# Kernel optimization log

Measured on AMD Instinct MI355X. Metric: run time of the kernel, lower is better.

## Reference

```python
import jax, jax.numpy as jnp
import numpy as np

B, N, D, H, S = 64, 1000, 512, 8, 20
DK = D // H
TANH_CLIP = 10.0
NEG = -1e9


def setup_inputs() -> dict:
    key = jax.random.key(0)
    k1, k2, k3, k4, k5 = jax.random.split(key, 5)
    embeddings = jax.random.normal(k1, (B, N, D), dtype=jnp.float32)
    q = jax.random.normal(k2, (B, S, D), dtype=jnp.float32)
    # action_mask: True = feasible. Ensure at least one feasible node per row.
    action_mask = jax.random.bernoulli(k3, 0.5, (B, S, N))
    action_mask = action_mask.at[:, :, 0].set(True)
    W_kvl = jax.random.normal(k4, (D, 3 * D), dtype=jnp.float32) * (1.0 / np.sqrt(D))
    W_out = jax.random.normal(k5, (D, D), dtype=jnp.float32) * (1.0 / np.sqrt(D))
    return {"embeddings": embeddings, "q": q, "action_mask": action_mask,
            "W_kvl": W_kvl, "W_out": W_out}


def reference(embeddings, q, action_mask, W_kvl, W_out):
    # _precompute: project node embeddings into glimpse K, V and logit K
    kvl = jnp.einsum('bnd,de->bne', embeddings, W_kvl)  # [B,N,3D]
    glimpse_k, glimpse_v, logit_k = jnp.split(kvl, 3, axis=-1)
    # dynamic embedding is zero (StaticEmbedding for TSP)

    mask = ~action_mask  # True = infeasible, shape [B,S,N]

    # multi-head glimpse attention
    qh = q.reshape(B, S, H, DK)
    kh = glimpse_k.reshape(B, N, H, DK)
    vh = glimpse_v.reshape(B, N, H, DK)
    compat = jnp.einsum('bshd,bnhd->bhsn', qh, kh) / np.sqrt(DK)
    compat = jnp.where(mask[:, None, :, :], NEG, compat)
    attn = jax.nn.softmax(compat, axis=-1)
    heads = jnp.einsum('bhsn,bnhd->bshd', attn, vh).reshape(B, S, D)
    glimpse = jnp.einsum('bsd,de->bse', heads, W_out)  # [B,S,D]

    # pointer logits against logit_k, tanh clipping, mask, log-softmax
    logits = jnp.einsum('bsd,bnd->bsn', glimpse, logit_k) / np.sqrt(D)
    logits = TANH_CLIP * jnp.tanh(logits)
    logits = jnp.where(mask, NEG, logits)
    log_p = jax.nn.log_softmax(logits, axis=-1)  # [B,S,N]

    # rearrange 'b s l -> (s b) l'
    return jnp.swapaxes(log_p, 0, 1).reshape(S * B, N)
```

## Files before the change

### kernel.cpp

```cpp
#include <hip/hip_runtime.h>

#define BB 64
#define NN 1000
#define NP 1024
#define DD 512
#define HH 8
#define SS 20
#define NEGV -1e9f

typedef float v4f __attribute__((ext_vector_type(4)));
typedef short v8s __attribute__((ext_vector_type(8)));
typedef int   v8i __attribute__((ext_vector_type(8)));
typedef int   v4i __attribute__((ext_vector_type(4)));
typedef unsigned char uchar;
typedef unsigned long long ulong_t;

static __device__ __forceinline__ short f2bf(float f) {
    unsigned u = __builtin_bit_cast(unsigned, f);
    u = (u + 0x7fffu + ((u >> 16) & 1u)) >> 16;
    return (short)u;
}
static __device__ __forceinline__ float bf2f(short s) {
    unsigned u = ((unsigned)(unsigned short)s) << 16;
    return __builtin_bit_cast(float, u);
}
static __device__ __forceinline__ uchar f2fp8(float f) {
    return (uchar)(__builtin_amdgcn_cvt_pk_fp8_f32(f, 0.f, 0, false) & 0xff);
}

static __device__ __forceinline__ void gld16(const void* g, void* l) {
    __builtin_amdgcn_global_load_lds(
        (const __attribute__((address_space(1))) void*)(g),
        (__attribute__((address_space(3))) void*)(l),
        16, 0, 0);
}

__global__ void transpose_bf16(const float* __restrict__ src, short* __restrict__ dst,
                               int R, int C) {
    __shared__ float t[32][33];
    int c0 = blockIdx.x * 32, r0 = blockIdx.y * 32;
    int x = threadIdx.x & 31, y = threadIdx.x >> 5;
    for (int k = 0; k < 32; k += 8)
        t[y + k][x] = src[(long)(r0 + y + k) * C + c0 + x];
    __syncthreads();
    for (int k = 0; k < 32; k += 8)
        dst[(long)(c0 + y + k) * R + r0 + x] = f2bf(t[x][y + k]);
}

__global__ void transpose_fp8(const float* __restrict__ src, uchar* __restrict__ dst,
                              int R, int C) {
    __shared__ float t[32][33];
    int c0 = blockIdx.x * 32, r0 = blockIdx.y * 32;
    int x = threadIdx.x & 31, y = threadIdx.x >> 5;
    for (int k = 0; k < 32; k += 8)
        t[y + k][x] = src[(long)(r0 + y + k) * C + c0 + x];
    __syncthreads();
    for (int k = 0; k < 32; k += 8)
        dst[(long)(c0 + y + k) * R + r0 + x] = f2fp8(t[x][y + k]);
}

__global__ void cvt_fp8(const float* __restrict__ src, int* __restrict__ dst, int n8) {
    int i = blockIdx.x * 256 + threadIdx.x;
    if (i >= n8) return;
    long o = (long)i * 8;
    v4f a = *(const v4f*)(src + o);
    v4f b = *(const v4f*)(src + o + 4);
    int lo = __builtin_amdgcn_cvt_pk_fp8_f32(a.x, a.y, 0, false);
    lo = __builtin_amdgcn_cvt_pk_fp8_f32(a.z, a.w, lo, true);
    int hi = __builtin_amdgcn_cvt_pk_fp8_f32(b.x, b.y, 0, false);
    hi = __builtin_amdgcn_cvt_pk_fp8_f32(b.z, b.w, hi, true);
    int2 r; r.x = lo; r.y = hi;
    *(int2*)(dst + i * 2) = r;
}

__global__ __launch_bounds__(256) void gemm_kvl(const uchar* __restrict__ emb8,
                                                const uchar* __restrict__ Wt8,
                                                uchar* __restrict__ kvl8) {
    __shared__ __align__(16) uchar As[128 * 128];
    __shared__ __align__(16) uchar Bs[128 * 128];
    __shared__ __align__(16) short rp[4 * 16 * 72];
    int tid = threadIdx.x;
    int id = blockIdx.x;
    int m_idx, n_idx;
    if (id < 5952) { int g = id / 96, r = id % 96; m_idx = g * 8 + (r & 7); n_idx = r >> 3; }
    else { int t = id - 5952; m_idx = 496 + (t & 3); n_idx = t >> 2; }
    int n0 = n_idx * 128, m0 = m_idx * 128;
    int wid = tid >> 6, lane = tid & 63, quad = lane >> 4, l16 = lane & 15;
    int wm = wid & 1, wn = wid >> 1;
    v4f acc[4][4] = {};
    const uchar* Ag = emb8 + (long)m0 * 512;
    const uchar* Bg = Wt8 + (long)n0 * 512;
    int rsub = lane >> 3;
    int kc = ((lane & 7) ^ rsub) * 16;
    for (int kk = 0; kk < 512; kk += 128) {
        #pragma unroll
        for (int p = 0; p < 4; ++p) {
            int rl = wid * 32 + p * 8;
            gld16(Ag + (long)(rl + rsub) * 512 + kk + kc, As + rl * 128);
            gld16(Bg + (long)(rl + rsub) * 512 + kk + kc, Bs + rl * 128);
        }
        __syncthreads();
        v8i af[4], bf[4];
        #pragma unroll
        for (int i = 0; i < 4; ++i) {
            int m = wm * 64 + i * 16 + l16;
            int c0 = (quad * 2) ^ (m & 7), c1 = (quad * 2 + 1) ^ (m & 7);
            v4i lo = *(const v4i*)(As + m * 128 + c0 * 16);
            v4i hi = *(const v4i*)(As + m * 128 + c1 * 16);
            af[i] = __builtin_shufflevector(lo, hi, 0, 1, 2, 3, 4, 5, 6, 7);
        }
        #pragma unroll
        for (int j = 0; j < 4; ++j) {
            int n = wn * 64 + j * 16 + l16;
            int c0 = (quad * 2) ^ (n & 7), c1 = (quad * 2 + 1) ^ (n & 7);
            v4i lo = *(const v4i*)(Bs + n * 128 + c0 * 16);
            v4i hi = *(const v4i*)(Bs + n * 128 + c1 * 16);
            bf[j] = __builtin_shufflevector(lo, hi, 0, 1, 2, 3, 4, 5, 6, 7);
        }
        #pragma unroll
        for (int i = 0; i < 4; ++i)
            #pragma unroll
            for (int j = 0; j < 4; ++j)
                acc[i][j] = __builtin_amdgcn_mfma_scale_f32_16x16x128_f8f6f4(
                    af[i], bf[j], acc[i][j], 0, 0, 0, 0x7f7f7f7f, 0, 0x7f7f7f7f);
        __syncthreads();
    }
    short* r = rp + wid * (16 * 72);
    #pragma unroll
    for (int i = 0; i < 4; ++i) {
        #pragma unroll
        for (int j = 0; j < 4; ++j)
            #pragma unroll
            for (int rr = 0; rr < 4; ++rr)
                r[(quad * 4 + rr) * 72 + j * 16 + l16] = f2bf(acc[i][j][rr]);
        #pragma unroll
        for (int h = 0; h < 2; ++h) {
            int rowl = h * 8 + (lane >> 3);
            int colc = (lane & 7) * 8;
            v8s val = *(const v8s*)(r + rowl * 72 + colc);
            int lo = __builtin_amdgcn_cvt_pk_fp8_f32(bf2f(val[0]), bf2f(val[1]), 0, false);
            lo = __builtin_amdgcn_cvt_pk_fp8_f32(bf2f(val[2]), bf2f(val[3]), lo, true);
            int hi = __builtin_amdgcn_cvt_pk_fp8_f32(bf2f(val[4]), bf2f(val[5]), 0, false);
            hi = __builtin_amdgcn_cvt_pk_fp8_f32(bf2f(val[6]), bf2f(val[7]), hi, true);
            int2 st; st.x = lo; st.y = hi;
            *(int2*)(kvl8 + (long)(m0 + wm * 64 + i * 16 + rowl) * 1536 +
                     n0 + wn * 64 + colc) = st;
        }
    }
}

__global__ void transpose_v(const uchar* __restrict__ kvl8, uchar* __restrict__ Vt8) {
    int bh = blockIdx.x, b = bh >> 3, h = bh & 7;
    int n0 = blockIdx.y * 64;
    __shared__ uchar T[64][72];
    int tid = threadIdx.x;
    #pragma unroll
    for (int it = 0; it < 2; ++it) {
        int nl = (tid >> 3) + it * 32;
        int n = n0 + nl;
        int nc = n < NN ? n : NN - 1;
        int d0 = (tid & 7) * 8;
        ulong_t v = *(const ulong_t*)(kvl8 + ((long)b * NN + nc) * 1536 + DD + h * 64 + d0);
        uchar* vb = (uchar*)&v;
        #pragma unroll
        for (int j = 0; j < 8; ++j) T[d0 + j][nl] = vb[j];
    }
    __syncthreads();
    #pragma unroll
    for (int it = 0; it < 2; ++it) {
        int d = (tid >> 3) + it * 32;
        int ns = (tid & 7) * 8;
        *(ulong_t*)(Vt8 + ((long)bh * 64 + d) * NP + n0 + ns) = *(const ulong_t*)&T[d][ns];
    }
}

#define CST 1036
__global__ __launch_bounds__(256) void attn_fused(const float* __restrict__ q,
                                                  const uchar* __restrict__ kvl8,
                                                  const uchar* __restrict__ Vt8,
                                                  const int* __restrict__ mask,
                                                  float* __restrict__ heads) {
    int b = blockIdx.x, h = blockIdx.y;
    __shared__ __align__(16) uchar qs[32 * 72];
    __shared__ __align__(16) short cmp[SS * CST];
    int tid = threadIdx.x, wid = tid >> 6, lane = tid & 63, quad = lane >> 4, l16 = lane & 15;
    for (int i = tid; i < 32 * 64; i += 256) {
        int row = i >> 6, col = i & 63;
        float v = (row < SS) ? q[((long)b * SS + row) * DD + h * 64 + col] : 0.f;
        qs[row * 72 + col] = f2fp8(v);
    }
    __syncthreads();
    long af[2][2];
    #pragma unroll
    for (int mt = 0; mt < 2; ++mt)
        #pragma unroll
        for (int ks = 0; ks < 2; ++ks)
            af[mt][ks] = *(const long*)(qs + (mt * 16 + l16) * 72 + ks * 32 + quad * 8);
    for (int t = 0; t < 16; ++t) {
        int nt = wid * 16 + t;
        int n = nt * 16 + l16;
        int nc = n < NN ? n : NN - 1;
        const uchar* kp = kvl8 + ((long)b * NN + nc) * 1536 + h * 64 + quad * 8;
        long b0 = *(const long*)kp;
        long b1 = *(const long*)(kp + 32);
        #pragma unroll
        for (int mt = 0; mt < 2; ++mt) {
            v4f a = {};
            a = __builtin_amdgcn_mfma_f32_16x16x32_fp8_fp8(af[mt][0], b0, a, 0, 0, 0);
            a = __builtin_amdgcn_mfma_f32_16x16x32_fp8_fp8(af[mt][1], b1, a, 0, 0, 0);
            #pragma unroll
            for (int r = 0; r < 4; ++r) {
                int s = mt * 16 + quad * 4 + r;
                if (s < SS) cmp[s * CST + nt * 16 + l16] = f2bf(a[r] * 0.125f);
            }
        }
    }
    __syncthreads();
    for (int s = wid; s < SS; s += 4) {
        const int* mr = mask + ((long)b * SS + s) * NN;
        float x[16];
        float mx = NEGV;
        #pragma unroll
        for (int i = 0; i < 16; ++i) {
            int n = lane + 64 * i;
            float v = bf2f(cmp[s * CST + n]);
            bool feas = (n < NN) && (mr[n < NN ? n : 0] != 0);
            x[i] = feas ? v : NEGV;
            mx = fmaxf(mx, x[i]);
        }
        for (int off = 32; off; off >>= 1) mx = fmaxf(mx, __shfl_xor(mx, off));
        float sum = 0.f;
        #pragma unroll
        for (int i = 0; i < 16; ++i) { x[i] = __expf(x[i] - mx); sum += x[i]; }
        for (int off = 32; off; off >>= 1) sum += __shfl_xor(sum, off);
        float inv = 1.0f / sum;
        uchar* pr = (uchar*)cmp + (long)s * (CST * 2);
        #pragma unroll
        for (int i = 0; i < 16; ++i) pr[lane + 64 * i] = f2fp8(x[i] * inv);
    }
    __syncthreads();
    int mt = wid & 1, dt0 = (wid >> 1) * 2;
    int srow = mt * 16 + l16; if (srow > SS - 1) srow = SS - 1;
    const uchar* ap = (const uchar*)cmp + (long)srow * (CST * 2) + quad * 8;
    const uchar* vb = Vt8 + (long)(b * HH + h) * 64 * NP;
    v4f acc[2] = {};
    for (int k0 = 0; k0 < NP; k0 += 32) {
        long afr = *(const long*)(ap + k0);
        #pragma unroll
        for (int i = 0; i < 2; ++i) {
            long bfr = *(const long*)(vb + (long)((dt0 + i) * 16 + l16) * NP + k0 + quad * 8);
            acc[i] = __builtin_amdgcn_mfma_f32_16x16x32_fp8_fp8(afr, bfr, acc[i], 0, 0, 0);
        }
    }
    #pragma unroll
    for (int i = 0; i < 2; ++i)
        #pragma unroll
        for (int r = 0; r < 4; ++r) {
            int s = mt * 16 + quad * 4 + r;
            if (s < SS)
                heads[((long)b * SS + s) * DD + h * 64 + (dt0 + i) * 16 + l16] = acc[i][r];
        }
}

__global__ __launch_bounds__(256) void out_proj(const float* __restrict__ heads,
                                                const short* __restrict__ Wot,
                                                float* __restrict__ glimpse) {
    __shared__ __align__(16) short As[64 * 40], Bs[64 * 40];
    int tid = threadIdx.x;
    int m0 = blockIdx.x * 64, n0 = blockIdx.y * 64;
    int wid = tid >> 6, lane = tid & 63, quad = lane >> 4, l16 = lane & 15;
    int wm = wid & 1, wn = wid >> 1;
    int arow = tid >> 3, akol = (tid & 7) * 4;
    int brow = tid >> 2, bkol = (tid & 3) * 8;
    v4f acc[2][2] = {};
    for (int kk = 0; kk < 512; kk += 32) {
        #pragma unroll
        for (int p = 0; p < 2; ++p) {
            int r = arow + p * 32;
            v4f a = *(const v4f*)(heads + (long)(m0 + r) * 512 + kk + akol);
            short4 s4;
            s4.x = f2bf(a.x); s4.y = f2bf(a.y); s4.z = f2bf(a.z); s4.w = f2bf(a.w);
            *(short4*)(As + r * 40 + akol) = s4;
        }
        *(uint4*)(Bs + brow * 40 + bkol) =
            *(const uint4*)(Wot + (long)(n0 + brow) * 512 + kk + bkol);
        __syncthreads();
        #pragma unroll
        for (int i = 0; i < 2; ++i) {
            v8s af = *(const v8s*)(As + (wm * 32 + i * 16 + l16) * 40 + quad * 8);
            #pragma unroll
            for (int j = 0; j < 2; ++j) {
                v8s bf = *(const v8s*)(Bs + (wn * 32 + j * 16 + l16) * 40 + quad * 8);
                acc[i][j] = __builtin_amdgcn_mfma_f32_16x16x32_bf16(af, bf, acc[i][j], 0, 0, 0);
            }
        }
        __syncthreads();
    }
    #pragma unroll
    for (int i = 0; i < 2; ++i)
        #pragma unroll
        for (int j = 0; j < 2; ++j)
            #pragma unroll
            for (int r = 0; r < 4; ++r)
                glimpse[(long)(m0 + wm * 32 + i * 16 + quad * 4 + r) * 512 +
                        n0 + wn * 32 + j * 16 + l16] = acc[i][j][r];
}

__global__ __launch_bounds__(256) void ptr_logits(const float* __restrict__ glimpse,
                                                  const uchar* __restrict__ kvl8,
                                                  float* __restrict__ logits) {
    int b = blockIdx.x, g = blockIdx.y;
    __shared__ __align__(16) uchar Gs[32 * 520];
    int tid = threadIdx.x;
    #pragma unroll
    for (int it = 0; it < 16; ++it) {
        int e = it * 1024 + tid * 4;
        int row = e >> 9, col = e & 511;
        int pk = 0;
        if (row < SS) {
            v4f a = *(const v4f*)(glimpse + ((long)b * SS + row) * 512 + col);
            pk = __builtin_amdgcn_cvt_pk_fp8_f32(a.x, a.y, 0, false);
            pk = __builtin_amdgcn_cvt_pk_fp8_f32(a.z, a.w, pk, true);
        }
        *(int*)(Gs + row * 520 + col) = pk;
    }
    __syncthreads();
    int wid = tid >> 6, lane = tid & 63, quad = lane >> 4, l16 = lane & 15;
    const float scale = 0.04419417382415922f;
    #pragma unroll
    for (int tc = 0; tc < 2; ++tc) {
        int nt = g * 8 + wid * 2 + tc;
        int n = nt * 16 + l16;
        int ncl = n < NN ? n : NN - 1;
        const uchar* kp = kvl8 + ((long)b * NN + ncl) * 1536 + 1024 + quad * 8;
        v4f acc[2] = {};
        for (int k = 0; k < 16; ++k) {
            long bfr = *(const long*)(kp + k * 32);
            #pragma unroll
            for (int m = 0; m < 2; ++m) {
                long afr = *(const long*)(Gs + (m * 16 + l16) * 520 + k * 32 + quad * 8);
                acc[m] = __builtin_amdgcn_mfma_f32_16x16x32_fp8_fp8(afr, bfr, acc[m], 0, 0, 0);
            }
        }
        #pragma unroll
        for (int m = 0; m < 2; ++m)
            #pragma unroll
            for (int r = 0; r < 4; ++r) {
                int s = m * 16 + quad * 4 + r;
                if (s < SS)
                    logits[((long)b * SS + s) * NP + nt * 16 + l16] = acc[m][r] * scale;
            }
    }
}

__global__ __launch_bounds__(256) void logsoftmax_out(const float* __restrict__ logits,
                                                      const int* __restrict__ mask,
                                                      float* __restrict__ out) {
    int row = blockIdx.x;
    int b = row / SS, s = row % SS;
    int tid = threadIdx.x;
    __shared__ float red[8];
    int n0 = tid * 4;
    v4f v = *(const v4f*)(logits + (long)row * NP + n0);
    const int* mr = mask + (long)row * NN;
    float x[4];
    float mx = NEGV;
    #pragma unroll
    for (int j = 0; j < 4; ++j) {
        int n = n0 + j;
        float t = 10.f * tanhf(v[j]);
        bool feas = (n < NN) && (mr[n < NN ? n : 0] != 0);
        x[j] = feas ? t : NEGV;
        mx = fmaxf(mx, x[j]);
    }
    for (int off = 32; off; off >>= 1) mx = fmaxf(mx, __shfl_xor(mx, off));
    int wid = tid >> 6, lane = tid & 63;
    if (lane == 0) red[wid] = mx;
    __syncthreads();
    mx = fmaxf(fmaxf(red[0], red[1]), fmaxf(red[2], red[3]));
    float sum = 0.f;
    #pragma unroll
    for (int j = 0; j < 4; ++j) sum += __expf(x[j] - mx);
    for (int off = 32; off; off >>= 1) sum += __shfl_xor(sum, off);
    __syncthreads();
    if (lane == 0) red[4 + wid] = sum;
    __syncthreads();
    sum = red[4] + red[5] + red[6] + red[7];
    float lse = mx + __logf(sum);
    float* orow = out + ((long)s * BB + b) * NN;
    #pragma unroll
    for (int j = 0; j < 4; ++j) {
        int n = n0 + j;
        if (n < NN) orow[n] = x[j] - lse;
    }
}

extern "C" void kernel_launch(void* const* d_in, const int* in_sizes, int n_in,
                              void* d_out, int out_size, void* d_ws, size_t ws_size,
                              hipStream_t stream) {
    const float* emb  = (const float*)d_in[0];
    const float* q    = (const float*)d_in[1];
    const int*   mask = (const int*)d_in[2];
    const float* Wkvl = (const float*)d_in[3];
    const float* Wout = (const float*)d_in[4];
    float* out = (float*)d_out;

    char* ws = (char*)d_ws;
    uchar* kvl8    = (uchar*)ws; ws += (size_t)64000 * 1536;
    uchar* Vt8     = (uchar*)ws; ws += (size_t)512 * 64 * NP;
    uchar* Wt8     = (uchar*)ws; ws += (size_t)1536 * 512;
    uchar* emb8    = (uchar*)ws; ws += (size_t)64000 * 512;
    short* Wot     = (short*)ws; ws += (size_t)512 * 512 * 2;
    float* heads   = (float*)ws; ws += (size_t)BB * SS * DD * 4;
    float* glimpse = (float*)ws; ws += (size_t)BB * SS * DD * 4;
    float* logits  = (float*)ws; ws += (size_t)BB * SS * NP * 4;

    transpose_fp8<<<dim3(48, 16), 256, 0, stream>>>(Wkvl, Wt8, 512, 1536);
    transpose_bf16<<<dim3(16, 16), 256, 0, stream>>>(Wout, Wot, 512, 512);
    cvt_fp8<<<dim3(16000), 256, 0, stream>>>(emb, (int*)emb8, 64000 * 512 / 8);
    gemm_kvl<<<dim3(6000), 256, 0, stream>>>(emb8, Wt8, kvl8);
    transpose_v<<<dim3(512, 16), 256, 0, stream>>>(kvl8, Vt8);
    attn_fused<<<dim3(BB, HH), 256, 0, stream>>>(q, kvl8, Vt8, mask, heads);
    out_proj<<<dim3(20, 8), 256, 0, stream>>>(heads, Wot, glimpse);
    ptr_logits<<<dim3(BB, 8), 256, 0, stream>>>(glimpse, kvl8, logits);
    logsoftmax_out<<<dim3(BB * SS), 256, 0, stream>>>(logits, mask, out);
}
```

Measured before the change: 360.0 us.

## Merge prep kernels, reuse GEMM LDS, double attention and logits parallelism

Combines the two weight-transpose kernels and the embedding fp8 conversion into one launch to cut launch overhead. The GEMM epilogue staging buffer now aliases the A tile in shared memory instead of taking its own allocation. The attention kernel uses 512 threads with half the per-wave work, and the pointer-logits kernel uses twice as many blocks with one n-tile per wave. Together these raise occupancy and parallelism on the small kernels, at the cost of more blocks each loading the shared Q or glimpse tile.

```diff
diff --git a/kernel.cpp b/kernel.cpp
--- a/kernel.cpp
+++ b/kernel.cpp
@@ -35,42 +35,40 @@
         16, 0, 0);
 }
 
-__global__ void transpose_bf16(const float* __restrict__ src, short* __restrict__ dst,
-                               int R, int C) {
+__global__ void prep(const float* __restrict__ Wkvl, uchar* __restrict__ Wt8,
+                     const float* __restrict__ Wout, short* __restrict__ Wot,
+                     const float* __restrict__ emb, int* __restrict__ emb8) {
     __shared__ float t[32][33];
-    int c0 = blockIdx.x * 32, r0 = blockIdx.y * 32;
-    int x = threadIdx.x & 31, y = threadIdx.x >> 5;
-    for (int k = 0; k < 32; k += 8)
-        t[y + k][x] = src[(long)(r0 + y + k) * C + c0 + x];
-    __syncthreads();
-    for (int k = 0; k < 32; k += 8)
-        dst[(long)(c0 + y + k) * R + r0 + x] = f2bf(t[x][y + k]);
-}
-
-__global__ void transpose_fp8(const float* __restrict__ src, uchar* __restrict__ dst,
-                              int R, int C) {
-    __shared__ float t[32][33];
-    int c0 = blockIdx.x * 32, r0 = blockIdx.y * 32;
-    int x = threadIdx.x & 31, y = threadIdx.x >> 5;
-    for (int k = 0; k < 32; k += 8)
-        t[y + k][x] = src[(long)(r0 + y + k) * C + c0 + x];
-    __syncthreads();
-    for (int k = 0; k < 32; k += 8)
-        dst[(long)(c0 + y + k) * R + r0 + x] = f2fp8(t[x][y + k]);
-}
-
-__global__ void cvt_fp8(const float* __restrict__ src, int* __restrict__ dst, int n8) {
-    int i = blockIdx.x * 256 + threadIdx.x;
-    if (i >= n8) return;
-    long o = (long)i * 8;
-    v4f a = *(const v4f*)(src + o);
-    v4f b = *(const v4f*)(src + o + 4);
-    int lo = __builtin_amdgcn_cvt_pk_fp8_f32(a.x, a.y, 0, false);
-    lo = __builtin_amdgcn_cvt_pk_fp8_f32(a.z, a.w, lo, true);
-    int hi = __builtin_amdgcn_cvt_pk_fp8_f32(b.x, b.y, 0, false);
-    hi = __builtin_amdgcn_cvt_pk_fp8_f32(b.z, b.w, hi, true);
-    int2 r; r.x = lo; r.y = hi;
-    *(int2*)(dst + i * 2) = r;
+    int bid = blockIdx.x, tid = threadIdx.x;
+    if (bid < 768) {
+        int c0 = (bid % 48) * 32, r0 = (bid / 48) * 32;
+        int x = tid & 31, y = tid >> 5;
+        for (int k = 0; k < 32; k += 8)
+            t[y + k][x] = Wkvl[(long)(r0 + y + k) * 1536 + c0 + x];
+        __syncthreads();
+        for (int k = 0; k < 32; k += 8)
+            Wt8[(long)(c0 + y + k) * 512 + r0 + x] = f2fp8(t[x][y + k]);
+    } else if (bid < 1024) {
+        int bb = bid - 768;
+        int c0 = (bb & 15) * 32, r0 = (bb >> 4) * 32;
+        int x = tid & 31, y = tid >> 5;
+        for (int k = 0; k < 32; k += 8)
+            t[y + k][x] = Wout[(long)(r0 + y + k) * 512 + c0 + x];
+        __syncthreads();
+        for (int k = 0; k < 32; k += 8)
+            Wot[(long)(c0 + y + k) * 512 + r0 + x] = f2bf(t[x][y + k]);
+    } else {
+        int i = (bid - 1024) * 256 + tid;
+        long o = (long)i * 8;
+        v4f a = *(const v4f*)(emb + o);
+        v4f b = *(const v4f*)(emb + o + 4);
+        int lo = __builtin_amdgcn_cvt_pk_fp8_f32(a.x, a.y, 0, false);
+        lo = __builtin_amdgcn_cvt_pk_fp8_f32(a.z, a.w, lo, true);
+        int hi = __builtin_amdgcn_cvt_pk_fp8_f32(b.x, b.y, 0, false);
+        hi = __builtin_amdgcn_cvt_pk_fp8_f32(b.z, b.w, hi, true);
+        int2 r; r.x = lo; r.y = hi;
+        *(int2*)(emb8 + i * 2) = r;
+    }
 }
 
 __global__ __launch_bounds__(256) void gemm_kvl(const uchar* __restrict__ emb8,
@@ -78,7 +76,6 @@
                                                 uchar* __restrict__ kvl8) {
     __shared__ __align__(16) uchar As[128 * 128];
     __shared__ __align__(16) uchar Bs[128 * 128];
-    __shared__ __align__(16) short rp[4 * 16 * 72];
     int tid = threadIdx.x;
     int id = blockIdx.x;
     int m_idx, n_idx;
@@ -125,6 +122,7 @@
                     af[i], bf[j], acc[i][j], 0, 0, 0, 0x7f7f7f7f, 0, 0x7f7f7f7f);
         __syncthreads();
     }
+    short* rp = (short*)As;
     short* r = rp + wid * (16 * 72);
     #pragma unroll
     for (int i = 0; i < 4; ++i) {
@@ -175,7 +173,7 @@
 }
 
 #define CST 1036
-__global__ __launch_bounds__(256) void attn_fused(const float* __restrict__ q,
+__global__ __launch_bounds__(512) void attn_fused(const float* __restrict__ q,
                                                   const uchar* __restrict__ kvl8,
                                                   const uchar* __restrict__ Vt8,
                                                   const int* __restrict__ mask,
@@ -184,7 +182,7 @@
     __shared__ __align__(16) uchar qs[32 * 72];
     __shared__ __align__(16) short cmp[SS * CST];
     int tid = threadIdx.x, wid = tid >> 6, lane = tid & 63, quad = lane >> 4, l16 = lane & 15;
-    for (int i = tid; i < 32 * 64; i += 256) {
+    for (int i = tid; i < 32 * 64; i += 512) {
         int row = i >> 6, col = i & 63;
         float v = (row < SS) ? q[((long)b * SS + row) * DD + h * 64 + col] : 0.f;
         qs[row * 72 + col] = f2fp8(v);
@@ -196,8 +194,8 @@
         #pragma unroll
         for (int ks = 0; ks < 2; ++ks)
             af[mt][ks] = *(const long*)(qs + (mt * 16 + l16) * 72 + ks * 32 + quad * 8);
-    for (int t = 0; t < 16; ++t) {
-        int nt = wid * 16 + t;
+    for (int t = 0; t < 8; ++t) {
+        int nt = wid * 8 + t;
         int n = nt * 16 + l16;
         int nc = n < NN ? n : NN - 1;
         const uchar* kp = kvl8 + ((long)b * NN + nc) * 1536 + h * 64 + quad * 8;
@@ -216,7 +214,7 @@
         }
     }
     __syncthreads();
-    for (int s = wid; s < SS; s += 4) {
+    for (int s = wid; s < SS; s += 8) {
         const int* mr = mask + ((long)b * SS + s) * NN;
         float x[16];
         float mx = NEGV;
@@ -239,27 +237,22 @@
         for (int i = 0; i < 16; ++i) pr[lane + 64 * i] = f2fp8(x[i] * inv);
     }
     __syncthreads();
-    int mt = wid & 1, dt0 = (wid >> 1) * 2;
+    int mt = wid & 1, dt = wid >> 1;
     int srow = mt * 16 + l16; if (srow > SS - 1) srow = SS - 1;
     const uchar* ap = (const uchar*)cmp + (long)srow * (CST * 2) + quad * 8;
     const uchar* vb = Vt8 + (long)(b * HH + h) * 64 * NP;
-    v4f acc[2] = {};
+    v4f acc = {};
     for (int k0 = 0; k0 < NP; k0 += 32) {
         long afr = *(const long*)(ap + k0);
-        #pragma unroll
-        for (int i = 0; i < 2; ++i) {
-            long bfr = *(const long*)(vb + (long)((dt0 + i) * 16 + l16) * NP + k0 + quad * 8);
-            acc[i] = __builtin_amdgcn_mfma_f32_16x16x32_fp8_fp8(afr, bfr, acc[i], 0, 0, 0);
-        }
-    }
-    #pragma unroll
-    for (int i = 0; i < 2; ++i)
-        #pragma unroll
-        for (int r = 0; r < 4; ++r) {
-            int s = mt * 16 + quad * 4 + r;
-            if (s < SS)
-                heads[((long)b * SS + s) * DD + h * 64 + (dt0 + i) * 16 + l16] = acc[i][r];
-        }
+        long bfr = *(const long*)(vb + (long)(dt * 16 + l16) * NP + k0 + quad * 8);
+        acc = __builtin_amdgcn_mfma_f32_16x16x32_fp8_fp8(afr, bfr, acc, 0, 0, 0);
+    }
+    #pragma unroll
+    for (int r = 0; r < 4; ++r) {
+        int s = mt * 16 + quad * 4 + r;
+        if (s < SS)
+            heads[((long)b * SS + s) * DD + h * 64 + dt * 16 + l16] = acc[r];
+    }
 }
 
 __global__ __launch_bounds__(256) void out_proj(const float* __restrict__ heads,
@@ -327,30 +320,27 @@
     __syncthreads();
     int wid = tid >> 6, lane = tid & 63, quad = lane >> 4, l16 = lane & 15;
     const float scale = 0.04419417382415922f;
-    #pragma unroll
-    for (int tc = 0; tc < 2; ++tc) {
-        int nt = g * 8 + wid * 2 + tc;
-        int n = nt * 16 + l16;
-        int ncl = n < NN ? n : NN - 1;
-        const uchar* kp = kvl8 + ((long)b * NN + ncl) * 1536 + 1024 + quad * 8;
-        v4f acc[2] = {};
-        for (int k = 0; k < 16; ++k) {
-            long bfr = *(const long*)(kp + k * 32);
-            #pragma unroll
-            for (int m = 0; m < 2; ++m) {
-                long afr = *(const long*)(Gs + (m * 16 + l16) * 520 + k * 32 + quad * 8);
-                acc[m] = __builtin_amdgcn_mfma_f32_16x16x32_fp8_fp8(afr, bfr, acc[m], 0, 0, 0);
-            }
-        }
-        #pragma unroll
-        for (int m = 0; m < 2; ++m)
-            #pragma unroll
-            for (int r = 0; r < 4; ++r) {
-                int s = m * 16 + quad * 4 + r;
-                if (s < SS)
-                    logits[((long)b * SS + s) * NP + nt * 16 + l16] = acc[m][r] * scale;
-            }
-    }
+    int nt = g * 4 + wid;
+    int n = nt * 16 + l16;
+    int ncl = n < NN ? n : NN - 1;
+    const uchar* kp = kvl8 + ((long)b * NN + ncl) * 1536 + 1024 + quad * 8;
+    v4f acc[2] = {};
+    for (int k = 0; k < 16; ++k) {
+        long bfr = *(const long*)(kp + k * 32);
+        #pragma unroll
+        for (int m = 0; m < 2; ++m) {
+            long afr = *(const long*)(Gs + (m * 16 + l16) * 520 + k * 32 + quad * 8);
+            acc[m] = __builtin_amdgcn_mfma_f32_16x16x32_fp8_fp8(afr, bfr, acc[m], 0, 0, 0);
+        }
+    }
+    #pragma unroll
+    for (int m = 0; m < 2; ++m)
+        #pragma unroll
+        for (int r = 0; r < 4; ++r) {
+            int s = m * 16 + quad * 4 + r;
+            if (s < SS)
+                logits[((long)b * SS + s) * NP + nt * 16 + l16] = acc[m][r] * scale;
+        }
 }
 
 __global__ __launch_bounds__(256) void logsoftmax_out(const float* __restrict__ logits,
@@ -415,13 +405,11 @@
     float* glimpse = (float*)ws; ws += (size_t)BB * SS * DD * 4;
     float* logits  = (float*)ws; ws += (size_t)BB * SS * NP * 4;
 
-    transpose_fp8<<<dim3(48, 16), 256, 0, stream>>>(Wkvl, Wt8, 512, 1536);
-    transpose_bf16<<<dim3(16, 16), 256, 0, stream>>>(Wout, Wot, 512, 512);
-    cvt_fp8<<<dim3(16000), 256, 0, stream>>>(emb, (int*)emb8, 64000 * 512 / 8);
+    prep<<<dim3(1024 + 16000), 256, 0, stream>>>(Wkvl, Wt8, Wout, Wot, emb, (int*)emb8);
     gemm_kvl<<<dim3(6000), 256, 0, stream>>>(emb8, Wt8, kvl8);
     transpose_v<<<dim3(512, 16), 256, 0, stream>>>(kvl8, Vt8);
-    attn_fused<<<dim3(BB, HH), 256, 0, stream>>>(q, kvl8, Vt8, mask, heads);
+    attn_fused<<<dim3(BB, HH), 512, 0, stream>>>(q, kvl8, Vt8, mask, heads);
     out_proj<<<dim3(20, 8), 256, 0, stream>>>(heads, Wot, glimpse);
-    ptr_logits<<<dim3(BB, 8), 256, 0, stream>>>(glimpse, kvl8, logits);
+    ptr_logits<<<dim3(BB, 16), 256, 0, stream>>>(glimpse, kvl8, logits);
     logsoftmax_out<<<dim3(BB * SS), 256, 0, stream>>>(logits, mask, out);
 }
```

Measured after the change: 351.7 us. 1.02x faster.
